# Performance work log

Measured on AMD Instinct MI355X. Metric: run time of the kernel, lower is better.

## Reference

```python
import jax, jax.numpy as jnp
import numpy as np

K = 3          # opt.k: number of nearest SOM nodes each point is assigned to
SOM_M = 256    # opt.node_num (16x16 SOM grid)


def _point_resnet(x, ws, bs):
    # SO-Net PointResNet: stack of 1x1 conv (relu) layers; the LAST layer takes
    # concat(prev_out, input) as a residual skip connection.
    out = x
    n = len(ws)
    for i in range(n):
        inp = jnp.concatenate([out, x], axis=1) if i == n - 1 else out
        out = jax.nn.relu(jnp.einsum('oc,bcn->bon', ws[i], inp) + bs[i][None, :, None])
    return out


def _encoder(x, sn, node, fp_ws, fp_bs, fn_ws, fn_bs):
    B, _, N = x.shape
    M = node.shape[2]
    xd = jax.lax.stop_gradient(x)      # torch used x.data throughout SOM logic
    nd = jax.lax.stop_gradient(node)
    # squared distances point->node: B,N,M
    x2 = jnp.sum(xd * xd, axis=1)
    n2 = jnp.sum(nd * nd, axis=1)
    cross = jnp.einsum('bcn,bcm->bnm', xd, nd)
    d2 = x2[:, :, None] + n2[:, None, :] - 2.0 * cross
    _, knn_idx = jax.lax.top_k(-d2, K)                 # B,N,K nearest SOM nodes
    min_idx = jnp.transpose(knn_idx, (0, 2, 1)).reshape(B, K * N)  # B,kN (k-major, matches x_stack)
    x_stack = jnp.tile(x, (1, 1, K))                   # B,3,kN
    xs_d = jax.lax.stop_gradient(x_stack)
    # mask_row_sum (counts per node) and masked sum == one-hot mask multiply in the original
    counts = jax.vmap(lambda s: jax.ops.segment_sum(jnp.ones(s.shape, jnp.float32), s, num_segments=SOM_M))(min_idx)  # B,M
    sums = jax.vmap(lambda d, s: jax.ops.segment_sum(d, s, num_segments=SOM_M))(jnp.transpose(xs_d, (0, 2, 1)), min_idx)  # B,M,3
    cluster_mean = jnp.transpose(sums, (0, 2, 1)) / (counts[:, None, :] + 1e-5)  # B,3,M (new som_node)
    # centers: per-point gather of its assigned node (sum(mask*node) over M)
    centers = jnp.take_along_axis(cluster_mean, min_idx[:, None, :], axis=2)     # B,3,kN
    x_dec = jax.lax.stop_gradient(x_stack - centers)   # .detach() in original
    first = _point_resnet(x_dec, fp_ws, fp_bs)         # B,384,kN
    # index_max + gather: per (b,c,node) max over assigned points; empty nodes -> point index 0
    node_max = jax.vmap(lambda d, s: jax.ops.segment_max(d, s, num_segments=SOM_M))(jnp.transpose(first, (0, 2, 1)), min_idx)  # B,M,C
    node_max = jnp.transpose(node_max, (0, 2, 1))      # B,C,M
    has_pts = counts > 0                               # mask_row_max
    fallback = first[:, :, 0:1]                        # gather index 0 for empty nodes
    masked_max = jnp.where(has_pts[:, None, :], node_max, fallback)  # B,384,M
    final_in = jnp.concatenate([cluster_mean, masked_max], axis=1)   # B,387,M
    final = _point_resnet(final_in, fn_ws, fn_bs)      # B,1024,M
    return jnp.max(final, axis=2)                      # B,1024 global feature


def setup_inputs() -> dict:
    key = jax.random.key(0)
    ks = jax.random.split(key, 24)
    B, N, M = 8, 4096, SOM_M
    inp = {
        'x': jax.random.normal(ks[0], (B, 3, N), jnp.float32),
        'sn': jax.random.normal(ks[1], (B, 3, N), jnp.float32),
        'node': jax.random.normal(ks[2], (B, 3, M), jnp.float32),
        'node_knn_I': jax.random.randint(ks[3], (B, M, 1), 0, M),
    }
    fp_dims = [(3, 64), (64, 128), (128, 256), (256 + 3, 384)]
    fn_dims = [(387, 512), (512, 512), (512, 768), (768 + 387, 1024)]
    i = 4
    for j, (cin, cout) in enumerate(fp_dims):
        inp[f'fp_w{j}'] = jax.random.normal(ks[i], (cout, cin), jnp.float32) * np.float32(np.sqrt(2.0 / cin)); i += 1
        inp[f'fp_b{j}'] = jnp.zeros((cout,), jnp.float32)
    for j, (cin, cout) in enumerate(fn_dims):
        inp[f'fn_w{j}'] = jax.random.normal(ks[i], (cout, cin), jnp.float32) * np.float32(np.sqrt(2.0 / cin)); i += 1
        inp[f'fn_b{j}'] = jnp.zeros((cout,), jnp.float32)
    return inp


def reference(x, sn, node, node_knn_I,
              fp_w0, fp_b0, fp_w1, fp_b1, fp_w2, fp_b2, fp_w3, fp_b3,
              fn_w0, fn_b0, fn_w1, fn_b1, fn_w2, fn_b2, fn_w3, fn_b3):
    fp_ws = [fp_w0, fp_w1, fp_w2, fp_w3]
    fp_bs = [fp_b0, fp_b1, fp_b2, fp_b3]
    fn_ws = [fn_w0, fn_w1, fn_w2, fn_w3]
    fn_bs = [fn_b0, fn_b1, fn_b2, fn_b3]
    # node_knn_I only used when som_k >= 2 (KNNModule); som_k=1 here.
    return _encoder(x, sn, node, fp_ws, fp_bs, fn_ws, fn_bs)
```

## Files before the change

kernel.cpp:

```cpp
#include <hip/hip_runtime.h>
#include <math.h>

#define B_   8
#define N_   4096
#define M_   256
#define KNN_ 3

#define OFF_COUNTS   0
#define OFF_SUMS     2048
#define OFF_CM       8192
#define OFF_NODEMAX  14336
#define OFF_FIRST0   800768
#define ZERO_COUNT   803840
#define OFF_KNN      807944
#define OFF_SORTED   906248
#define OFF_MSORT    1004552
#define OFF_WBF      2544648
#define OFF_W3X      3661832
#define O_W0 0
#define O_W1 2048
#define O_W2 10240
#define O_W3 43008
#define O_V0 153600
#define O_V1 366592
#define O_V2 628736
#define O_V3 1021952
#define W_TOTAL 2234368

typedef short  bf16x8 __attribute__((ext_vector_type(8)));
typedef float  f32x4  __attribute__((ext_vector_type(4)));
typedef float  f32x16 __attribute__((ext_vector_type(16)));

__device__ __forceinline__ unsigned short f2b(float f) {
    unsigned u = __float_as_uint(f);
    return (unsigned short)((u + 0x7FFFu + ((u >> 16) & 1u)) >> 16);
}
__device__ __forceinline__ unsigned cvt2(float lo, float hi) {
    unsigned r;
    asm("v_cvt_pk_bf16_f32 %0, %1, %2" : "=v"(r) : "v"(lo), "v"(hi));
    return r;
}
__device__ __forceinline__ f32x16 zero16() {
    f32x16 z;
    #pragma unroll
    for (int i = 0; i < 16; i++) z[i] = 0.f;
    return z;
}

__global__ __launch_bounds__(256) void knn_setup(
        const float* __restrict__ x, const float* __restrict__ node,
        int* __restrict__ knn, float* __restrict__ counts, float* __restrict__ sums,
        const float* s0, const float* s1, const float* s2, const float* s3,
        const float* s4, const float* s5, const float* s6, const float* s7,
        unsigned short* __restrict__ dst, float* __restrict__ w3x) {
    __shared__ float nd0[M_], nd1[M_], nd2[M_], nn2[M_];
    int t = threadIdx.x;
    if (blockIdx.x < 128) {
        int b = blockIdx.x >> 4, xblk = blockIdx.x & 15;
        {
            float c0 = node[(b * 3 + 0) * M_ + t];
            float c1 = node[(b * 3 + 1) * M_ + t];
            float c2 = node[(b * 3 + 2) * M_ + t];
            nd0[t] = c0; nd1[t] = c1; nd2[t] = c2;
            nn2[t] = c0 * c0 + c1 * c1 + c2 * c2;
        }
        __syncthreads();
        int n = xblk * 256 + t;
        float x0 = x[(b * 3 + 0) * N_ + n];
        float x1 = x[(b * 3 + 1) * N_ + n];
        float x2 = x[(b * 3 + 2) * N_ + n];
        float xx = x0 * x0 + x1 * x1 + x2 * x2;
        float d0 = 1e30f, d1 = 1e30f, d2b = 1e30f;
        int i0 = 0, i1 = 0, i2 = 0;
        for (int m = 0; m < M_; m++) {
            float cross = x0 * nd0[m] + x1 * nd1[m] + x2 * nd2[m];
            float d = xx + nn2[m] - 2.f * cross;
            bool c0 = d < d0, c1 = d < d1, c2 = d < d2b;
            d2b = c1 ? d1 : (c2 ? d : d2b);
            i2  = c1 ? i1 : (c2 ? m : i2);
            d1  = c0 ? d0 : (c1 ? d : d1);
            i1  = c0 ? i0 : (c1 ? m : i1);
            d0  = c0 ? d  : d0;
            i0  = c0 ? m  : i0;
        }
        int base = (b * N_ + n) * 3;
        knn[base + 0] = i0; knn[base + 1] = i1; knn[base + 2] = i2;
        int mm[3] = {i0, i1, i2};
        #pragma unroll
        for (int k = 0; k < 3; k++) {
            int m = mm[k];
            atomicAdd(&counts[b * M_ + m], 1.f);
            atomicAdd(&sums[(b * M_ + m) * 3 + 0], x0);
            atomicAdd(&sums[(b * M_ + m) * 3 + 1], x1);
            atomicAdd(&sums[(b * M_ + m) * 3 + 2], x2);
        }
    } else {
        int i = (blockIdx.x - 128) * 256 + t;
        int st = (gridDim.x - 128) * 256;
        for (int j = i; j < 1536; j += st) {
            int ch = j >> 2, c = j & 3;
            w3x[j] = (c < 3) ? s3[ch * 259 + 256 + c] : 0.f;
        }
        for (; i < W_TOTAL; i += st) {
            const float* src; int base, cin, cinp;
            if      (i < O_W1) { src = s0; base = O_W0; cin = 3;    cinp = 32; }
            else if (i < O_W2) { src = s1; base = O_W1; cin = 64;   cinp = 64; }
            else if (i < O_W3) { src = s2; base = O_W2; cin = 128;  cinp = 128; }
            else if (i < O_V0) { src = s3; base = O_W3; cin = 259;  cinp = 288; }
            else if (i < O_V1) { src = s4; base = O_V0; cin = 387;  cinp = 416; }
            else if (i < O_V2) { src = s5; base = O_V1; cin = 512;  cinp = 512; }
            else if (i < O_V3) { src = s6; base = O_V2; cin = 512;  cinp = 512; }
            else               { src = s7; base = O_V3; cin = 1155; cinp = 1184; }
            int loc = i - base;
            int co = loc / cinp, k = loc - co * cinp;
            dst[i] = (k < cin) ? f2b(src[co * cin + k]) : (unsigned short)0;
        }
    }
}

__global__ __launch_bounds__(256) void prep(const float* __restrict__ counts,
        const float* __restrict__ sums, const int* __restrict__ knn,
        float* __restrict__ cm, int* __restrict__ sorted, int* __restrict__ msort) {
    __shared__ int tmp[256], offsL[257], cur[256];
    int t = threadIdx.x, b = blockIdx.x;
    float cnt = counts[b * M_ + t];
    float inv = 1.f / (cnt + 1e-5f);
    #pragma unroll
    for (int c = 0; c < 3; c++)
        cm[(b * 3 + c) * M_ + t] = sums[(b * M_ + t) * 3 + c] * inv;
    int v = (int)cnt;
    tmp[t] = v; cur[t] = 0;
    __syncthreads();
    for (int off = 1; off < 256; off <<= 1) {
        int u = (t >= off) ? tmp[t - off] : 0;
        __syncthreads();
        tmp[t] += u;
        __syncthreads();
    }
    offsL[t] = tmp[t] - v;
    if (t == 255) offsL[256] = tmp[255];
    __syncthreads();
    for (int e = t; e < KNN_ * N_; e += 256) {
        int n = e & (N_ - 1), k = e >> 12;
        int m = knn[(b * N_ + n) * 3 + k];
        int pos = atomicAdd(&cur[m], 1);
        int dst = offsL[m] + pos;
        sorted[b * (KNN_ * N_) + dst] = e;
        msort[b * (KNN_ * N_) + dst] = m;
    }
}

template<int KS, int INS, int OUTS, int CTW>
__device__ __forceinline__ void layerB(const unsigned short* __restrict__ Wg,
        const float* __restrict__ bias, const unsigned short* actin,
        unsigned short* actout, int wave, int lane) {
    int r = lane & 15, g = lane >> 4;
    bf16x8 bfr[4][KS];
    #pragma unroll
    for (int pt = 0; pt < 4; pt++) {
        const unsigned short* arow = actin + (pt * 16 + r) * INS + g * 8;
        #pragma unroll
        for (int ks = 0; ks < KS; ks++)
            bfr[pt][ks] = *(const bf16x8*)(arow + ks * 32);
    }
    #pragma unroll
    for (int c = 0; c < CTW; c++) {
        int ct = wave * CTW + c;
        const unsigned short* wrow = Wg + (ct * 16 + r) * (KS * 32) + g * 8;
        f32x4 acc[4];
        #pragma unroll
        for (int pt = 0; pt < 4; pt++) acc[pt] = (f32x4){0.f, 0.f, 0.f, 0.f};
        #pragma unroll
        for (int ks = 0; ks < KS; ks++) {
            bf16x8 wv = *(const bf16x8*)(wrow + ks * 32);
            #pragma unroll
            for (int pt = 0; pt < 4; pt++)
                acc[pt] = __builtin_amdgcn_mfma_f32_16x16x32_bf16(wv, bfr[pt][ks], acc[pt], 0, 0, 0);
        }
        f32x4 b4 = *(const f32x4*)(bias + ct * 16 + g * 4);
        #pragma unroll
        for (int pt = 0; pt < 4; pt++) {
            uint2 s;
            s.x = cvt2(fmaxf(acc[pt][0] + b4[0], 0.f), fmaxf(acc[pt][1] + b4[1], 0.f));
            s.y = cvt2(fmaxf(acc[pt][2] + b4[2], 0.f), fmaxf(acc[pt][3] + b4[3], 0.f));
            *(uint2*)(actout + (pt * 16 + r) * OUTS + ct * 16 + g * 4) = s;
        }
    }
}

__global__ __launch_bounds__(256, 3) void mlp1m(
        const float* __restrict__ x, const float* __restrict__ cm,
        const int* __restrict__ sorted, const int* __restrict__ msort,
        const unsigned short* __restrict__ wb, const float4* __restrict__ w3x,
        const float* __restrict__ bb0, const float* __restrict__ bb1,
        const float* __restrict__ bb2, const float* __restrict__ bb3,
        float* __restrict__ node_max, float* __restrict__ first0) {
    __shared__ __align__(16) char smem[50688];
    unsigned short* inb = (unsigned short*)smem;
    unsigned short* a1  = (unsigned short*)smem;
    unsigned short* a0  = (unsigned short*)(smem + 16896);
    unsigned short* cat = (unsigned short*)(smem + 16896);
    __shared__ float4 xdf[64];
    __shared__ int segm[65], segstart[66];
    __shared__ int nseg, p0loc;
    int t = threadIdx.x, b = blockIdx.y, lane = t & 63, wave = t >> 6;
    int e0 = blockIdx.x * 64;
    for (int e = t; e < 1280; e += 256) ((unsigned*)inb)[e] = 0u;
    __syncthreads();
    if (t < 64) {
        int p = t;
        if (p == 0) p0loc = -1;
        int j = sorted[b * 12288 + e0 + p];
        int m = msort[b * 12288 + e0 + p];
        int n = j & (N_ - 1);
        float xd0 = x[(b * 3 + 0) * N_ + n] - cm[(b * 3 + 0) * M_ + m];
        float xd1 = x[(b * 3 + 1) * N_ + n] - cm[(b * 3 + 1) * M_ + m];
        float xd2 = x[(b * 3 + 2) * N_ + n] - cm[(b * 3 + 2) * M_ + m];
        xdf[p] = make_float4(xd0, xd1, xd2, 0.f);
        inb[p * 40 + 0] = f2b(xd0);
        inb[p * 40 + 1] = f2b(xd1);
        inb[p * 40 + 2] = f2b(xd2);
        int prev = __shfl_up(m, 1);
        bool flag = (p == 0) || (m != prev);
        unsigned long long mk = __ballot(flag);
        int sid = __popcll(mk & ((1ull << p) - 1ull));
        if (flag) { segstart[sid] = p; segm[sid] = m; }
        if (p == 63) { int ns2 = __popcll(mk); nseg = ns2; segstart[ns2] = 64; }
        if (j == 0) p0loc = p;
    }
    __syncthreads();
    layerB<1, 40, 72, 1>(wb + O_W0, bb0, inb, a0, wave, lane);
    __syncthreads();
    layerB<2, 72, 132, 2>(wb + O_W1, bb1, a0, a1, wave, lane);
    __syncthreads();
    layerB<4, 132, 264, 4>(wb + O_W2, bb2, a1, cat, wave, lane);
    __syncthreads();
    int l31 = lane & 31, half = lane >> 5;
    f32x16 acc[6];
    #pragma unroll
    for (int q = 0; q < 6; q++) acc[q] = zero16();
    {
        const unsigned short* arow0 = cat + l31 * 264 + half * 8;
        const unsigned short* arow1 = cat + (32 + l31) * 264 + half * 8;
        const unsigned short* wrowb = wb + O_W3 + (wave * 96 + l31) * 288 + half * 8;
        #pragma unroll
        for (int ks = 0; ks < 16; ks++) {
            bf16x8 aA = *(const bf16x8*)(arow0 + ks * 16);
            bf16x8 aB = *(const bf16x8*)(arow1 + ks * 16);
            #pragma unroll
            for (int c3 = 0; c3 < 3; c3++) {
                bf16x8 wv = *(const bf16x8*)(wrowb + c3 * 32 * 288 + ks * 16);
                acc[c3 * 2 + 0] = __builtin_amdgcn_mfma_f32_32x32x16_bf16(aA, wv, acc[c3 * 2 + 0], 0, 0, 0);
                acc[c3 * 2 + 1] = __builtin_amdgcn_mfma_f32_32x32x16_bf16(aB, wv, acc[c3 * 2 + 1], 0, 0, 0);
            }
        }
    }
    int ns = nseg, p0l = p0loc;
    float bias3[3]; float4 wx3[3];
    #pragma unroll
    for (int c3 = 0; c3 < 3; c3++) {
        bias3[c3] = bb3[(wave * 3 + c3) * 32 + l31];
        wx3[c3]   = w3x[(wave * 3 + c3) * 32 + l31];
    }
    #pragma unroll
    for (int ph = 0; ph < 2; ph++) {
        #pragma unroll
        for (int rg = 0; rg < 16; rg++) {
            int row = ph * 32 + (rg & 3) + 8 * (rg >> 2) + 4 * half;
            float4 xv = xdf[row];
            #pragma unroll
            for (int c3 = 0; c3 < 3; c3++) {
                float s = acc[c3 * 2 + ph][rg] + bias3[c3]
                        + wx3[c3].x * xv.x + wx3[c3].y * xv.y + wx3[c3].z * xv.z;
                acc[c3 * 2 + ph][rg] = fmaxf(s, 0.f);
            }
        }
    }
    if (p0l >= 0) {
        #pragma unroll
        for (int ph = 0; ph < 2; ph++)
            #pragma unroll
            for (int rg = 0; rg < 16; rg++) {
                int row = ph * 32 + (rg & 3) + 8 * (rg >> 2) + 4 * half;
                if (row == p0l) {
                    #pragma unroll
                    for (int c3 = 0; c3 < 3; c3++)
                        first0[b * 384 + (wave * 3 + c3) * 32 + l31] = acc[c3 * 2 + ph][rg];
                }
            }
    }
    for (int s = 0; s < ns; s++) {
        int s0 = segstart[s], s1 = segstart[s + 1];
        float m0 = 0.f, m1 = 0.f, m2 = 0.f;
        if (s0 < 32) {
            #pragma unroll
            for (int rg = 0; rg < 16; rg++) {
                int row = (rg & 3) + 8 * (rg >> 2) + 4 * half;
                bool in = (row >= s0) && (row < s1);
                m0 = fmaxf(m0, in ? acc[0][rg] : 0.f);
                m1 = fmaxf(m1, in ? acc[2][rg] : 0.f);
                m2 = fmaxf(m2, in ? acc[4][rg] : 0.f);
            }
        }
        if (s1 > 32) {
            #pragma unroll
            for (int rg = 0; rg < 16; rg++) {
                int row = 32 + (rg & 3) + 8 * (rg >> 2) + 4 * half;
                bool in = (row >= s0) && (row < s1);
                m0 = fmaxf(m0, in ? acc[1][rg] : 0.f);
                m1 = fmaxf(m1, in ? acc[3][rg] : 0.f);
                m2 = fmaxf(m2, in ? acc[5][rg] : 0.f);
            }
        }
        m0 = fmaxf(m0, __shfl_xor(m0, 32));
        m1 = fmaxf(m1, __shfl_xor(m1, 32));
        m2 = fmaxf(m2, __shfl_xor(m2, 32));
        if (lane < 32) {
            float* dstp = &node_max[(size_t)(b * M_ + segm[s]) * 384 + wave * 96];
            atomicMax((int*)(dstp + l31),      __float_as_int(m0));
            atomicMax((int*)(dstp + 32 + l31), __float_as_int(m1));
            atomicMax((int*)(dstp + 64 + l31), __float_as_int(m2));
        }
    }
}

__global__ __launch_bounds__(1024) void node_mlp(
        const float* __restrict__ cm, const float* __restrict__ counts,
        const float* __restrict__ nmax, const float* __restrict__ first0,
        const unsigned short* __restrict__ wb,
        const float* __restrict__ q0, const float* __restrict__ q1,
        const float* __restrict__ q2, const float* __restrict__ q3,
        float* __restrict__ out) {
    __shared__ __align__(16) char smem[71424];
    unsigned short* cat = (unsigned short*)smem;
    unsigned short* h0  = (unsigned short*)(smem + 38144);
    unsigned short* h1  = (unsigned short*)(smem + 54784);
    int t = threadIdx.x, lane = t & 63, w = t >> 6;
    int nt = blockIdx.x, b = nt >> 4;
    for (int e = t; e < 16 * 424; e += 1024) {
        int nl = e / 424, ch = e - nl * 424;
        int ng = nt * 16 + nl, m = ng & 255;
        float v = 0.f;
        if (ch < 3) v = cm[(b * 3 + ch) * M_ + m];
        else if (ch < 387)
            v = (counts[ng] > 0.f) ? nmax[(size_t)ng * 384 + (ch - 3)]
                                   : first0[b * 384 + (ch - 3)];
        cat[nl * 1192 + 768 + ch] = f2b(v);
    }
    __syncthreads();
    int r = lane & 15, g = lane >> 4;
    {
        bf16x8 afr[13];
        const unsigned short* arow = cat + r * 1192 + 768 + g * 8;
        #pragma unroll
        for (int ks = 0; ks < 13; ks++) afr[ks] = *(const bf16x8*)(arow + ks * 32);
        f32x4 acc[2] = {{0.f,0.f,0.f,0.f}, {0.f,0.f,0.f,0.f}};
        const unsigned short* w0 = wb + O_V0 + ((w * 2) * 16 + r) * 416 + g * 8;
        #pragma unroll
        for (int ks = 0; ks < 13; ks++) {
            #pragma unroll
            for (int c = 0; c < 2; c++)
                acc[c] = __builtin_amdgcn_mfma_f32_16x16x32_bf16(
                    *(const bf16x8*)(w0 + c * 16 * 416 + ks * 32), afr[ks], acc[c], 0, 0, 0);
        }
        #pragma unroll
        for (int c = 0; c < 2; c++) {
            int ct = w * 2 + c;
            f32x4 b4 = *(const f32x4*)(q0 + ct * 16 + g * 4);
            uint2 s;
            s.x = cvt2(fmaxf(acc[c][0] + b4[0], 0.f), fmaxf(acc[c][1] + b4[1], 0.f));
            s.y = cvt2(fmaxf(acc[c][2] + b4[2], 0.f), fmaxf(acc[c][3] + b4[3], 0.f));
            *(uint2*)(h0 + r * 520 + ct * 16 + g * 4) = s;
        }
    }
    __syncthreads();
    {
        bf16x8 afr[16];
        const unsigned short* arow = h0 + r * 520 + g * 8;
        #pragma unroll
        for (int ks = 0; ks < 16; ks++) afr[ks] = *(const bf16x8*)(arow + ks * 32);
        f32x4 acc[2] = {{0.f,0.f,0.f,0.f}, {0.f,0.f,0.f,0.f}};
        const unsigned short* w0 = wb + O_V1 + ((w * 2) * 16 + r) * 512 + g * 8;
        #pragma unroll
        for (int ks = 0; ks < 16; ks++) {
            #pragma unroll
            for (int c = 0; c < 2; c++)
                acc[c] = __builtin_amdgcn_mfma_f32_16x16x32_bf16(
                    *(const bf16x8*)(w0 + c * 16 * 512 + ks * 32), afr[ks], acc[c], 0, 0, 0);
        }
        #pragma unroll
        for (int c = 0; c < 2; c++) {
            int ct = w * 2 + c;
            f32x4 b4 = *(const f32x4*)(q1 + ct * 16 + g * 4);
            uint2 s;
            s.x = cvt2(fmaxf(acc[c][0] + b4[0], 0.f), fmaxf(acc[c][1] + b4[1], 0.f));
            s.y = cvt2(fmaxf(acc[c][2] + b4[2], 0.f), fmaxf(acc[c][3] + b4[3], 0.f));
            *(uint2*)(h1 + r * 520 + ct * 16 + g * 4) = s;
        }
    }
    __syncthreads();
    {
        bf16x8 afr[16];
        const unsigned short* arow = h1 + r * 520 + g * 8;
        #pragma unroll
        for (int ks = 0; ks < 16; ks++) afr[ks] = *(const bf16x8*)(arow + ks * 32);
        f32x4 acc[3] = {{0.f,0.f,0.f,0.f}, {0.f,0.f,0.f,0.f}, {0.f,0.f,0.f,0.f}};
        const unsigned short* w0 = wb + O_V2 + ((w * 3) * 16 + r) * 512 + g * 8;
        #pragma unroll
        for (int ks = 0; ks < 16; ks++) {
            #pragma unroll
            for (int c = 0; c < 3; c++)
                acc[c] = __builtin_amdgcn_mfma_f32_16x16x32_bf16(
                    *(const bf16x8*)(w0 + c * 16 * 512 + ks * 32), afr[ks], acc[c], 0, 0, 0);
        }
        #pragma unroll
        for (int c = 0; c < 3; c++) {
            int ct = w * 3 + c;
            f32x4 b4 = *(const f32x4*)(q2 + ct * 16 + g * 4);
            uint2 s;
            s.x = cvt2(fmaxf(acc[c][0] + b4[0], 0.f), fmaxf(acc[c][1] + b4[1], 0.f));
            s.y = cvt2(fmaxf(acc[c][2] + b4[2], 0.f), fmaxf(acc[c][3] + b4[3], 0.f));
            *(uint2*)(cat + r * 1192 + ct * 16 + g * 4) = s;
        }
    }
    __syncthreads();
    {
        f32x4 acc[4] = {{0.f,0.f,0.f,0.f}, {0.f,0.f,0.f,0.f},
                        {0.f,0.f,0.f,0.f}, {0.f,0.f,0.f,0.f}};
        const unsigned short* arow = cat + r * 1192 + g * 8;
        const unsigned short* w0 = wb + O_V3 + (size_t)((w * 4) * 16 + r) * 1184 + g * 8;
        #pragma unroll 4
        for (int ks = 0; ks < 37; ks++) {
            bf16x8 av = *(const bf16x8*)(arow + ks * 32);
            #pragma unroll
            for (int c = 0; c < 4; c++)
                acc[c] = __builtin_amdgcn_mfma_f32_16x16x32_bf16(
                    *(const bf16x8*)(w0 + (size_t)c * 16 * 1184 + ks * 32), av, acc[c], 0, 0, 0);
        }
        #pragma unroll
        for (int c = 0; c < 4; c++) {
            int ct = w * 4 + c;
            f32x4 b4 = *(const f32x4*)(q3 + ct * 16 + g * 4);
            #pragma unroll
            for (int i = 0; i < 4; i++) {
                float v = fmaxf(acc[c][i] + b4[i], 0.f);
                v = fmaxf(v, __shfl_xor(v, 1));
                v = fmaxf(v, __shfl_xor(v, 2));
                v = fmaxf(v, __shfl_xor(v, 4));
                v = fmaxf(v, __shfl_xor(v, 8));
                if (r == 0)
                    atomicMax((int*)&out[b * 1024 + ct * 16 + g * 4 + i],
                              __float_as_int(v));
            }
        }
    }
}

extern "C" void kernel_launch(void* const* d_in, const int* in_sizes, int n_in,
                              void* d_out, int out_size, void* d_ws, size_t ws_size,
                              hipStream_t stream) {
    (void)in_sizes; (void)n_in; (void)out_size; (void)ws_size;
    const float* x    = (const float*)d_in[0];
    const float* node = (const float*)d_in[2];
    const float* fpw[4] = {(const float*)d_in[4], (const float*)d_in[6],
                           (const float*)d_in[8], (const float*)d_in[10]};
    const float* fpb[4] = {(const float*)d_in[5], (const float*)d_in[7],
                           (const float*)d_in[9], (const float*)d_in[11]};
    const float* fnw[4] = {(const float*)d_in[12], (const float*)d_in[14],
                           (const float*)d_in[16], (const float*)d_in[18]};
    const float* fnb[4] = {(const float*)d_in[13], (const float*)d_in[15],
                           (const float*)d_in[17], (const float*)d_in[19]};
    float* ws  = (float*)d_ws;
    float* out = (float*)d_out;
    unsigned short* wb = (unsigned short*)(ws + OFF_WBF);

    hipMemsetAsync(ws, 0, (size_t)ZERO_COUNT * 4, stream);
    hipMemsetAsync(out, 0, (size_t)B_ * 1024 * 4, stream);

    knn_setup<<<128 + 2048, 256, 0, stream>>>(
        x, node, (int*)(ws + OFF_KNN), ws + OFF_COUNTS, ws + OFF_SUMS,
        fpw[0], fpw[1], fpw[2], fpw[3], fnw[0], fnw[1], fnw[2], fnw[3],
        wb, ws + OFF_W3X);
    prep<<<B_, 256, 0, stream>>>(
        ws + OFF_COUNTS, ws + OFF_SUMS, (int*)(ws + OFF_KNN),
        ws + OFF_CM, (int*)(ws + OFF_SORTED), (int*)(ws + OFF_MSORT));
    mlp1m<<<dim3(KNN_ * N_ / 64, B_), 256, 0, stream>>>(
        x, ws + OFF_CM, (int*)(ws + OFF_SORTED), (int*)(ws + OFF_MSORT), wb,
        (const float4*)(ws + OFF_W3X),
        fpb[0], fpb[1], fpb[2], fpb[3], ws + OFF_NODEMAX, ws + OFF_FIRST0);
    node_mlp<<<128, 1024, 0, stream>>>(
        ws + OFF_CM, ws + OFF_COUNTS, ws + OFF_NODEMAX, ws + OFF_FIRST0, wb,
        fnb[0], fnb[1], fnb[2], fnb[3], out);
}
```

Before: 225.9 us.

## Split node MLP into 8-node blocks to fill all CUs; specialize weight conversion

Result: no change. 225.8 us (-0.1%).

```diff
diff --git a/kernel.cpp b/kernel.cpp
--- a/kernel.cpp
+++ b/kernel.cpp
@@ -102,18 +102,33 @@
             w3x[j] = (c < 3) ? s3[ch * 259 + 256 + c] : 0.f;
         }
         for (; i < W_TOTAL; i += st) {
-            const float* src; int base, cin, cinp;
-            if      (i < O_W1) { src = s0; base = O_W0; cin = 3;    cinp = 32; }
-            else if (i < O_W2) { src = s1; base = O_W1; cin = 64;   cinp = 64; }
-            else if (i < O_W3) { src = s2; base = O_W2; cin = 128;  cinp = 128; }
-            else if (i < O_V0) { src = s3; base = O_W3; cin = 259;  cinp = 288; }
-            else if (i < O_V1) { src = s4; base = O_V0; cin = 387;  cinp = 416; }
-            else if (i < O_V2) { src = s5; base = O_V1; cin = 512;  cinp = 512; }
-            else if (i < O_V3) { src = s6; base = O_V2; cin = 512;  cinp = 512; }
-            else               { src = s7; base = O_V3; cin = 1155; cinp = 1184; }
-            int loc = i - base;
-            int co = loc / cinp, k = loc - co * cinp;
-            dst[i] = (k < cin) ? f2b(src[co * cin + k]) : (unsigned short)0;
+            unsigned short v;
+            if (i < O_W1) {
+                int loc = i, co = loc >> 5, k = loc & 31;
+                v = (k < 3) ? f2b(s0[co * 3 + k]) : (unsigned short)0;
+            } else if (i < O_W2) {
+                int loc = i - O_W1, co = loc >> 6, k = loc & 63;
+                v = f2b(s1[co * 64 + k]);
+            } else if (i < O_W3) {
+                int loc = i - O_W2, co = loc >> 7, k = loc & 127;
+                v = f2b(s2[co * 128 + k]);
+            } else if (i < O_V0) {
+                int loc = i - O_W3, co = loc / 288u, k = loc - co * 288;
+                v = (k < 259) ? f2b(s3[co * 259 + k]) : (unsigned short)0;
+            } else if (i < O_V1) {
+                int loc = i - O_V0, co = loc / 416u, k = loc - co * 416;
+                v = (k < 387) ? f2b(s4[co * 387 + k]) : (unsigned short)0;
+            } else if (i < O_V2) {
+                int loc = i - O_V1, co = loc >> 9, k = loc & 511;
+                v = f2b(s5[co * 512 + k]);
+            } else if (i < O_V3) {
+                int loc = i - O_V2, co = loc >> 9, k = loc & 511;
+                v = f2b(s6[co * 512 + k]);
+            } else {
+                int loc = i - O_V3, co = loc / 1184u, k = loc - co * 1184;
+                v = (k < 1155) ? f2b(s7[co * 1155 + k]) : (unsigned short)0;
+            }
+            dst[i] = v;
         }
     }
 }
@@ -324,22 +339,22 @@
     }
 }
 
-__global__ __launch_bounds__(1024) void node_mlp(
+__global__ __launch_bounds__(512) void node_mlp(
         const float* __restrict__ cm, const float* __restrict__ counts,
         const float* __restrict__ nmax, const float* __restrict__ first0,
         const unsigned short* __restrict__ wb,
         const float* __restrict__ q0, const float* __restrict__ q1,
         const float* __restrict__ q2, const float* __restrict__ q3,
         float* __restrict__ out) {
-    __shared__ __align__(16) char smem[71424];
+    __shared__ __align__(16) char smem[35712];
     unsigned short* cat = (unsigned short*)smem;
-    unsigned short* h0  = (unsigned short*)(smem + 38144);
-    unsigned short* h1  = (unsigned short*)(smem + 54784);
+    unsigned short* h0  = (unsigned short*)(smem + 19072);
+    unsigned short* h1  = (unsigned short*)(smem + 27392);
     int t = threadIdx.x, lane = t & 63, w = t >> 6;
-    int nt = blockIdx.x, b = nt >> 4;
-    for (int e = t; e < 16 * 424; e += 1024) {
+    int nt = blockIdx.x, b = nt >> 5;
+    for (int e = t; e < 8 * 424; e += 512) {
         int nl = e / 424, ch = e - nl * 424;
-        int ng = nt * 16 + nl, m = ng & 255;
+        int ng = nt * 8 + nl, m = ng & 255;
         float v = 0.f;
         if (ch < 3) v = cm[(b * 3 + ch) * M_ + m];
         else if (ch < 387)
@@ -348,98 +363,94 @@
         cat[nl * 1192 + 768 + ch] = f2b(v);
     }
     __syncthreads();
-    int r = lane & 15, g = lane >> 4;
+    int r = lane & 15, g = lane >> 4, r8 = r & 7;
     {
-        bf16x8 afr[13];
-        const unsigned short* arow = cat + r * 1192 + 768 + g * 8;
-        #pragma unroll
-        for (int ks = 0; ks < 13; ks++) afr[ks] = *(const bf16x8*)(arow + ks * 32);
-        f32x4 acc[2] = {{0.f,0.f,0.f,0.f}, {0.f,0.f,0.f,0.f}};
-        const unsigned short* w0 = wb + O_V0 + ((w * 2) * 16 + r) * 416 + g * 8;
+        const unsigned short* arow = cat + r8 * 1192 + 768 + g * 8;
+        const unsigned short* w0 = wb + O_V0 + ((w * 4) * 16 + r) * 416 + g * 8;
+        f32x4 acc[4] = {{0.f,0.f,0.f,0.f},{0.f,0.f,0.f,0.f},{0.f,0.f,0.f,0.f},{0.f,0.f,0.f,0.f}};
         #pragma unroll
         for (int ks = 0; ks < 13; ks++) {
-            #pragma unroll
-            for (int c = 0; c < 2; c++)
+            bf16x8 av = *(const bf16x8*)(arow + ks * 32);
+            #pragma unroll
+            for (int c = 0; c < 4; c++)
                 acc[c] = __builtin_amdgcn_mfma_f32_16x16x32_bf16(
-                    *(const bf16x8*)(w0 + c * 16 * 416 + ks * 32), afr[ks], acc[c], 0, 0, 0);
-        }
-        #pragma unroll
-        for (int c = 0; c < 2; c++) {
-            int ct = w * 2 + c;
+                    *(const bf16x8*)(w0 + c * 16 * 416 + ks * 32), av, acc[c], 0, 0, 0);
+        }
+        #pragma unroll
+        for (int c = 0; c < 4; c++) {
+            int ct = w * 4 + c;
             f32x4 b4 = *(const f32x4*)(q0 + ct * 16 + g * 4);
             uint2 s;
             s.x = cvt2(fmaxf(acc[c][0] + b4[0], 0.f), fmaxf(acc[c][1] + b4[1], 0.f));
             s.y = cvt2(fmaxf(acc[c][2] + b4[2], 0.f), fmaxf(acc[c][3] + b4[3], 0.f));
-            *(uint2*)(h0 + r * 520 + ct * 16 + g * 4) = s;
+            if (r < 8) *(uint2*)(h0 + r * 520 + ct * 16 + g * 4) = s;
         }
     }
     __syncthreads();
     {
-        bf16x8 afr[16];
-        const unsigned short* arow = h0 + r * 520 + g * 8;
-        #pragma unroll
-        for (int ks = 0; ks < 16; ks++) afr[ks] = *(const bf16x8*)(arow + ks * 32);
-        f32x4 acc[2] = {{0.f,0.f,0.f,0.f}, {0.f,0.f,0.f,0.f}};
-        const unsigned short* w0 = wb + O_V1 + ((w * 2) * 16 + r) * 512 + g * 8;
+        const unsigned short* arow = h0 + r8 * 520 + g * 8;
+        const unsigned short* w0 = wb + O_V1 + ((w * 4) * 16 + r) * 512 + g * 8;
+        f32x4 acc[4] = {{0.f,0.f,0.f,0.f},{0.f,0.f,0.f,0.f},{0.f,0.f,0.f,0.f},{0.f,0.f,0.f,0.f}};
         #pragma unroll
         for (int ks = 0; ks < 16; ks++) {
-            #pragma unroll
-            for (int c = 0; c < 2; c++)
+            bf16x8 av = *(const bf16x8*)(arow + ks * 32);
+            #pragma unroll
+            for (int c = 0; c < 4; c++)
                 acc[c] = __builtin_amdgcn_mfma_f32_16x16x32_bf16(
-                    *(const bf16x8*)(w0 + c * 16 * 512 + ks * 32), afr[ks], acc[c], 0, 0, 0);
-        }
-        #pragma unroll
-        for (int c = 0; c < 2; c++) {
-            int ct = w * 2 + c;
+                    *(const bf16x8*)(w0 + c * 16 * 512 + ks * 32), av, acc[c], 0, 0, 0);
+        }
+        #pragma unroll
+        for (int c = 0; c < 4; c++) {
+            int ct = w * 4 + c;
             f32x4 b4 = *(const f32x4*)(q1 + ct * 16 + g * 4);
             uint2 s;
             s.x = cvt2(fmaxf(acc[c][0] + b4[0], 0.f), fmaxf(acc[c][1] + b4[1], 0.f));
             s.y = cvt2(fmaxf(acc[c][2] + b4[2], 0.f), fmaxf(acc[c][3] + b4[3], 0.f));
-            *(uint2*)(h1 + r * 520 + ct * 16 + g * 4) = s;
+            if (r < 8) *(uint2*)(h1 + r * 520 + ct * 16 + g * 4) = s;
         }
     }
     __syncthreads();
     {
-        bf16x8 afr[16];
-        const unsigned short* arow = h1 + r * 520 + g * 8;
-        #pragma unroll
-        for (int ks = 0; ks < 16; ks++) afr[ks] = *(const bf16x8*)(arow + ks * 32);
-        f32x4 acc[3] = {{0.f,0.f,0.f,0.f}, {0.f,0.f,0.f,0.f}, {0.f,0.f,0.f,0.f}};
-        const unsigned short* w0 = wb + O_V2 + ((w * 3) * 16 + r) * 512 + g * 8;
+        const unsigned short* arow = h1 + r8 * 520 + g * 8;
+        const unsigned short* w0 = wb + O_V2 + ((w * 6) * 16 + r) * 512 + g * 8;
+        f32x4 acc[6] = {{0.f,0.f,0.f,0.f},{0.f,0.f,0.f,0.f},{0.f,0.f,0.f,0.f},
+                        {0.f,0.f,0.f,0.f},{0.f,0.f,0.f,0.f},{0.f,0.f,0.f,0.f}};
         #pragma unroll
         for (int ks = 0; ks < 16; ks++) {
-            #pragma unroll
-            for (int c = 0; c < 3; c++)
+            bf16x8 av = *(const bf16x8*)(arow + ks * 32);
+            #pragma unroll
+            for (int c = 0; c < 6; c++)
                 acc[c] = __builtin_amdgcn_mfma_f32_16x16x32_bf16(
-                    *(const bf16x8*)(w0 + c * 16 * 512 + ks * 32), afr[ks], acc[c], 0, 0, 0);
-        }
-        #pragma unroll
-        for (int c = 0; c < 3; c++) {
-            int ct = w * 3 + c;
+                    *(const bf16x8*)(w0 + c * 16 * 512 + ks * 32), av, acc[c], 0, 0, 0);
+        }
+        #pragma unroll
+        for (int c = 0; c < 6; c++) {
+            int ct = w * 6 + c;
             f32x4 b4 = *(const f32x4*)(q2 + ct * 16 + g * 4);
             uint2 s;
             s.x = cvt2(fmaxf(acc[c][0] + b4[0], 0.f), fmaxf(acc[c][1] + b4[1], 0.f));
             s.y = cvt2(fmaxf(acc[c][2] + b4[2], 0.f), fmaxf(acc[c][3] + b4[3], 0.f));
-            *(uint2*)(cat + r * 1192 + ct * 16 + g * 4) = s;
+            if (r < 8) *(uint2*)(cat + r * 1192 + ct * 16 + g * 4) = s;
         }
     }
     __syncthreads();
     {
-        f32x4 acc[4] = {{0.f,0.f,0.f,0.f}, {0.f,0.f,0.f,0.f},
-                        {0.f,0.f,0.f,0.f}, {0.f,0.f,0.f,0.f}};
-        const unsigned short* arow = cat + r * 1192 + g * 8;
-        const unsigned short* w0 = wb + O_V3 + (size_t)((w * 4) * 16 + r) * 1184 + g * 8;
+        const unsigned short* arow = cat + r8 * 1192 + g * 8;
+        const unsigned short* w0 = wb + O_V3 + (size_t)((w * 8) * 16 + r) * 1184 + g * 8;
+        f32x4 acc[8];
+        #pragma unroll
+        for (int c = 0; c < 8; c++) acc[c] = (f32x4){0.f, 0.f, 0.f, 0.f};
         #pragma unroll 4
         for (int ks = 0; ks < 37; ks++) {
             bf16x8 av = *(const bf16x8*)(arow + ks * 32);
             #pragma unroll
-            for (int c = 0; c < 4; c++)
+            for (int c = 0; c < 8; c++)
                 acc[c] = __builtin_amdgcn_mfma_f32_16x16x32_bf16(
                     *(const bf16x8*)(w0 + (size_t)c * 16 * 1184 + ks * 32), av, acc[c], 0, 0, 0);
         }
         #pragma unroll
-        for (int c = 0; c < 4; c++) {
-            int ct = w * 4 + c;
+        for (int c = 0; c < 8; c++) {
+            int ct = w * 8 + c;
             f32x4 b4 = *(const f32x4*)(q3 + ct * 16 + g * 4);
             #pragma unroll
             for (int i = 0; i < 4; i++) {
@@ -488,7 +499,7 @@
         x, ws + OFF_CM, (int*)(ws + OFF_SORTED), (int*)(ws + OFF_MSORT), wb,
         (const float4*)(ws + OFF_W3X),
         fpb[0], fpb[1], fpb[2], fpb[3], ws + OFF_NODEMAX, ws + OFF_FIRST0);
-    node_mlp<<<128, 1024, 0, stream>>>(
+    node_mlp<<<256, 512, 0, stream>>>(
         ws + OFF_CM, ws + OFF_COUNTS, ws + OFF_NODEMAX, ws + OFF_FIRST0, wb,
         fnb[0], fnb[1], fnb[2], fnb[3], out);
 }
```
